# Kernel optimization log

Hardware: AMD Instinct MI355X
Metric: run time of the kernel (lower is better)

Reference implementation:

```python
import jax, jax.numpy as jnp
import numpy as np

HEADS = 16
D_MODEL = 1024
MAX_LEN = 1024
BATCH = 4
SEQ = 1024


def _skew(QEr):
    # Transformer-XL / Music-Transformer skew trick.
    # QEr: [B, H, L, L] -> pad one zero column on the left, reshape, drop first row.
    B, H, L, _ = QEr.shape
    padded = jnp.pad(QEr, ((0, 0), (0, 0), (0, 0), (1, 0)))  # [B,H,L,L+1]
    reshaped = padded.reshape(B, H, L + 1, L)
    return reshaped[:, :, 1:, :]  # [B,H,L,L]


def setup_inputs() -> dict:
    key = jax.random.key(0)
    ks = jax.random.split(key, 8)
    d = D_MODEL // HEADS
    std = 0.05  # tf.random_normal_initializer default stddev
    return {
        "query": jax.random.normal(ks[0], (BATCH, SEQ, D_MODEL), jnp.float32),
        "key": jax.random.normal(ks[1], (BATCH, SEQ, D_MODEL), jnp.float32),
        "value": jax.random.normal(ks[2], (BATCH, SEQ, D_MODEL), jnp.float32),
        "WQ": std * jax.random.normal(ks[3], (D_MODEL, D_MODEL), jnp.float32),
        "WK": std * jax.random.normal(ks[4], (D_MODEL, D_MODEL), jnp.float32),
        "WV": std * jax.random.normal(ks[5], (D_MODEL, D_MODEL), jnp.float32),
        "Er": std * jax.random.normal(ks[6], (MAX_LEN, d), jnp.float32),
        "WMerge": std * jax.random.normal(ks[7], (D_MODEL, D_MODEL), jnp.float32),
    }


def reference(query, key, value, WQ, WK, WV, Er, WMerge):
    B, L, D = query.shape
    H = HEADS
    d = D // H
    # Faithful to source: plain reshape (NOT transpose-based head split).
    q = (query @ WQ).reshape(B, H, L, d)          # [B,H,L,d]
    k_t = (key @ WK).reshape(B, H, d, L)          # [B,H,d,L]
    v = (value @ WV).reshape(B, H, L, d)          # [B,H,L,d]
    start = MAX_LEN - L
    Er_t = Er[start:, :].T                        # [d, L]
    QEr = q @ Er_t                                # [B,H,L,L]
    Srel = _skew(QEr)                             # [B,H,L,L]
    attn = (q @ k_t + Srel) / jnp.sqrt(jnp.asarray(d, q.dtype))
    attn = jax.nn.softmax(attn, axis=-1)
    out = attn @ v                                # [B,H,L,d]
    out = out.transpose(0, 2, 1, 3).reshape(B, L, D)
    return out @ WMerge
```

## Files before the change

### kernel.cpp

```cpp
#include <hip/hip_runtime.h>

#define H_  16
#define L_  1024
#define D_  1024
#define DH  64

typedef short bf16x8 __attribute__((ext_vector_type(8)));
typedef float f32x4  __attribute__((ext_vector_type(4)));

__device__ __forceinline__ ushort f2bf(float f) {
  union { float f; unsigned int u; } x; x.f = f;
  unsigned int u = x.u;
  u = (u + 0x7fffu + ((u >> 16) & 1u)) >> 16;
  return (ushort)u;
}
__device__ __forceinline__ float bf2f(ushort s) {
  union { unsigned int u; float f; } x; x.u = ((unsigned int)s) << 16;
  return x.f;
}

__device__ __forceinline__ unsigned int pkbf(float a, float b) {
  union { float f; unsigned int u; } xa, xb; xa.f = a; xb.f = b;
  unsigned int ua = xa.u + 0x8000u;
  unsigned int ub = xb.u + 0x8000u;
  return (ua >> 16) | (ub & 0xffff0000u);
}
__device__ __forceinline__ ushort lo16(unsigned int v) { return (ushort)v; }
__device__ __forceinline__ ushort hi16(unsigned int v) { return (ushort)(v >> 16); }

__device__ __forceinline__ int SZ(int F) { return F ^ (((F >> 12) & 3) << 4); }

__device__ __forceinline__ size_t afi(int m, int k) {
  return (((size_t)((m >> 7) * 32 + (k >> 5)) * 8 + ((m >> 4) & 7)) << 9)
       + ((size_t)((((k >> 3) & 3) << 4) + (m & 15)) << 3) + (k & 7);
}

__device__ __forceinline__ void gl_lds16(const ushort* g, ushort* l) {
  __builtin_amdgcn_global_load_lds(
      (const __attribute__((address_space(1))) void*)g,
      (__attribute__((address_space(3))) void*)l, 16, 0, 0);
}

__global__ __launch_bounds__(256) void prep_kernel(
    const float* __restrict__ q, const float* __restrict__ k, const float* __restrict__ v,
    ushort* __restrict__ qb, ushort* __restrict__ kb, ushort* __restrict__ vb,
    const float* __restrict__ W0, const float* __restrict__ W1,
    const float* __restrict__ W2, const float* __restrict__ W3,
    ushort* __restrict__ T0, ushort* __restrict__ T1,
    ushort* __restrict__ T2, ushort* __restrict__ T3,
    const float* __restrict__ Er, ushort* __restrict__ ErF) {
  const int bx = blockIdx.x;
  const int tid = threadIdx.x;
  if (bx < 6144) {
    const int z = bx >> 11;
    const int inner = bx & 2047;
    const float* in = (z == 0) ? q : (z == 1) ? k : v;
    ushort* out = (z == 0) ? qb : (z == 1) ? kb : vb;
    const int wv = inner * 4 + (tid >> 6);
    const int l  = tid & 63;
    const int am = wv & 7, kb2 = (wv >> 3) & 31, mb = wv >> 8;
    const int m  = mb * 128 + am * 16 + (l & 15);
    const int kk = kb2 * 32 + (l >> 4) * 8;
    float4 f0 = *(const float4*)(in + (size_t)m * 1024 + kk);
    float4 f1 = *(const float4*)(in + (size_t)m * 1024 + kk + 4);
    uint4 o;
    o.x = pkbf(f0.x, f0.y); o.y = pkbf(f0.z, f0.w);
    o.z = pkbf(f1.x, f1.y); o.w = pkbf(f1.z, f1.w);
    *(uint4*)(out + ((size_t)wv << 9) + l * 8) = o;
  } else if (bx < 7168) {
    __shared__ ushort tt[64][72];
    const int b = bx - 6144;
    const int z = b >> 8;
    const int rem = b & 255;
    const int k0 = (rem >> 4) * 64, n0 = (rem & 15) * 64;
    const float* W = (z == 0) ? W0 : (z == 1) ? W1 : (z == 2) ? W2 : W3;
    ushort*     WT = (z == 0) ? T0 : (z == 1) ? T1 : (z == 2) ? T2 : T3;
    const int t = tid;
#pragma unroll
    for (int c = 0; c < 4; ++c) {
      int kk = c * 16 + (t >> 4);
      float4 f = *(const float4*)(W + (size_t)(k0 + kk) * 1024 + n0 + (t & 15) * 4);
      unsigned int p01 = pkbf(f.x, f.y), p23 = pkbf(f.z, f.w);
      tt[(t & 15) * 4 + 0][kk] = lo16(p01);
      tt[(t & 15) * 4 + 1][kk] = hi16(p01);
      tt[(t & 15) * 4 + 2][kk] = lo16(p23);
      tt[(t & 15) * 4 + 3][kk] = hi16(p23);
    }
    __syncthreads();
#pragma unroll
    for (int p = 0; p < 2; ++p) {
      int n = p * 32 + (t >> 3);
      *(uint4*)(WT + afi(n0 + n, k0 + (t & 7) * 8)) = *(const uint4*)(&tt[n][(t & 7) * 8]);
    }
  } else {
    int t = (bx - 7168) * 256 + tid;
    int lane = t & 63, ph = (t >> 6) & 1, jg = t >> 7;
    int m = jg * 16 + (lane & 15);
    int kk = ph * 32 + (lane >> 4) * 8;
    float4 f0 = *(const float4*)(Er + m * 64 + kk);
    float4 f1 = *(const float4*)(Er + m * 64 + kk + 4);
    uint4 o;
    o.x = pkbf(f0.x, f0.y); o.y = pkbf(f0.z, f0.w);
    o.z = pkbf(f1.x, f1.y); o.w = pkbf(f1.z, f1.w);
    *(uint4*)(ErF + t * 8) = o;
  }
}

__global__ __launch_bounds__(256) void gemm_qkv_kernel(
    const ushort* __restrict__ Aq, const ushort* __restrict__ Ak, const ushort* __restrict__ Av,
    const ushort* __restrict__ BTq, const ushort* __restrict__ BTk, const ushort* __restrict__ BTv,
    ushort* __restrict__ Cq, ushort* __restrict__ Ck, ushort* __restrict__ Cv) {
  __shared__ ushort lsA[4096];
  __shared__ ushort lsB[4096];
  const int z = blockIdx.z;
  const ushort* A  = (z == 0) ? Aq  : (z == 1) ? Ak  : Av;
  const ushort* BT = (z == 0) ? BTq : (z == 1) ? BTk : BTv;
  ushort*       Cp = (z == 0) ? Cq  : (z == 1) ? Ck  : Cv;

  const int tid  = threadIdx.x;
  const int w    = tid >> 6, lane = tid & 63, qd = lane >> 4, ln = lane & 15;
  const int rw   = w >> 1, cw = w & 1;
  const int mb   = blockIdx.y, nb = blockIdx.x;
  const int m0   = mb * 128, n0 = nb * 128;

  f32x4 acc[16];
#pragma unroll
  for (int i = 0; i < 16; ++i) acc[i] = (f32x4){0.f, 0.f, 0.f, 0.f};

  for (int kb = 0; kb < 32; ++kb) {
    const ushort* Ab = A  + ((size_t)(mb * 32 + kb) << 12);
    const ushort* Bb = BT + ((size_t)(nb * 32 + kb) << 12);
    const int c0 = 2 * w;
    gl_lds16(Ab + ((size_t)c0 << 9) + lane * 8,        lsA + (c0 << 9));
    gl_lds16(Ab + ((size_t)(c0 + 1) << 9) + lane * 8,  lsA + ((c0 + 1) << 9));
    gl_lds16(Bb + ((size_t)c0 << 9) + lane * 8,        lsB + (c0 << 9));
    gl_lds16(Bb + ((size_t)(c0 + 1) << 9) + lane * 8,  lsB + ((c0 + 1) << 9));
    __syncthreads();
    bf16x8 afr[4], bfr[4];
#pragma unroll
    for (int am = 0; am < 4; ++am)
      afr[am] = *(const bf16x8*)(lsA + ((rw * 4 + am) << 9) + lane * 8);
#pragma unroll
    for (int bn = 0; bn < 4; ++bn)
      bfr[bn] = *(const bf16x8*)(lsB + ((cw * 4 + bn) << 9) + lane * 8);
#pragma unroll
    for (int am = 0; am < 4; ++am)
#pragma unroll
      for (int bn = 0; bn < 4; ++bn)
        acc[am * 4 + bn] = __builtin_amdgcn_mfma_f32_16x16x32_bf16(afr[am], bfr[bn], acc[am * 4 + bn], 0, 0, 0);
    __syncthreads();
  }
#pragma unroll
  for (int am = 0; am < 4; ++am)
#pragma unroll
    for (int bn = 0; bn < 4; ++bn) {
      const int rbase = m0 + rw * 64 + am * 16 + qd * 4;
      const int colg  = n0 + cw * 64 + bn * 16 + ln;
      const unsigned int p01 = pkbf(acc[am * 4 + bn][0], acc[am * 4 + bn][1]);
      const unsigned int p23 = pkbf(acc[am * 4 + bn][2], acc[am * 4 + bn][3]);
      if (z == 0) {
        Cp[(size_t)(rbase + 0) * 1024 + colg] = lo16(p01);
        Cp[(size_t)(rbase + 1) * 1024 + colg] = hi16(p01);
        Cp[(size_t)(rbase + 2) * 1024 + colg] = lo16(p23);
        Cp[(size_t)(rbase + 3) * 1024 + colg] = hi16(p23);
      } else if (z == 1) {
        const int bh  = rbase >> 6;
        const int ki0 = rbase & 63;
        const int jg  = colg >> 4;
        const int ph  = ki0 >> 5;
        const int lanep = ((ki0 >> 3) & 3) * 16 + (colg & 15);
        const int jj0 = ki0 & 7;
        uint2 uu; uu.x = p01; uu.y = p23;
        *(uint2*)(Cp + (size_t)bh * 65536 + (size_t)((jg * 2 + ph) * 64 + lanep) * 8 + jj0) = uu;
      } else {
        const int bh = rbase >> 6;
        const int llow = colg >> 6, dd = colg & 63;
        const int g = dd >> 4, lnf = dd & 15;
        const ushort vals[4] = {lo16(p01), hi16(p01), lo16(p23), hi16(p23)};
#pragma unroll
        for (int r = 0; r < 4; ++r) {
          int l = ((rbase + r) & 63) * 16 + llow;
          int ks = l >> 5;
          int lanep = ((l >> 3) & 3) * 16 + lnf;
          int jj = l & 7;
          Cp[(size_t)bh * 65536 + (size_t)((g * 32 + ks) * 64 + lanep) * 8 + jj] = vals[r];
        }
      }
    }
}

__global__ __launch_bounds__(256) void gemm_mg_kernel(const ushort* __restrict__ A,
                                                      const ushort* __restrict__ BT,
                                                      float* __restrict__ Cp) {
  __shared__ ushort lsA[4096];
  __shared__ ushort lsB[4096];
  const int tid  = threadIdx.x;
  const int w    = tid >> 6, lane = tid & 63, qd = lane >> 4, ln = lane & 15;
  const int rw   = w >> 1, cw = w & 1;
  const int mb   = blockIdx.y, nb = blockIdx.x, kh = blockIdx.z;
  const int m0   = mb * 128, n0 = nb * 128;

  f32x4 acc[16];
#pragma unroll
  for (int i = 0; i < 16; ++i) acc[i] = (f32x4){0.f, 0.f, 0.f, 0.f};

  for (int kb = 0; kb < 16; ++kb) {
    const int kbi = kh * 16 + kb;
    const ushort* Ab = A  + ((size_t)(mb * 32 + kbi) << 12);
    const ushort* Bb = BT + ((size_t)(nb * 32 + kbi) << 12);
    const int c0 = 2 * w;
    gl_lds16(Ab + ((size_t)c0 << 9) + lane * 8,        lsA + (c0 << 9));
    gl_lds16(Ab + ((size_t)(c0 + 1) << 9) + lane * 8,  lsA + ((c0 + 1) << 9));
    gl_lds16(Bb + ((size_t)c0 << 9) + lane * 8,        lsB + (c0 << 9));
    gl_lds16(Bb + ((size_t)(c0 + 1) << 9) + lane * 8,  lsB + ((c0 + 1) << 9));
    __syncthreads();
    bf16x8 afr[4], bfr[4];
#pragma unroll
    for (int am = 0; am < 4; ++am)
      afr[am] = *(const bf16x8*)(lsA + ((rw * 4 + am) << 9) + lane * 8);
#pragma unroll
    for (int bn = 0; bn < 4; ++bn)
      bfr[bn] = *(const bf16x8*)(lsB + ((cw * 4 + bn) << 9) + lane * 8);
#pragma unroll
    for (int am = 0; am < 4; ++am)
#pragma unroll
      for (int bn = 0; bn < 4; ++bn)
        acc[am * 4 + bn] = __builtin_amdgcn_mfma_f32_16x16x32_bf16(afr[am], bfr[bn], acc[am * 4 + bn], 0, 0, 0);
    __syncthreads();
  }

#pragma unroll
  for (int am = 0; am < 4; ++am)
#pragma unroll
    for (int bn = 0; bn < 4; ++bn) {
      const int rbase = m0 + rw * 64 + am * 16 + qd * 4;
      const int colg  = n0 + cw * 64 + bn * 16 + ln;
#pragma unroll
      for (int r = 0; r < 4; ++r)
        atomicAdd(&Cp[(size_t)(rbase + r) * 1024 + colg], acc[am * 4 + bn][r]);
    }
}

__global__ __launch_bounds__(512, 4) void attn_kernel(
    const ushort* __restrict__ QW, const ushort* __restrict__ KF,
    const ushort* __restrict__ VF, const ushort* __restrict__ ErF,
    ushort* __restrict__ Om) {
  __shared__ ushort qflat[17440];
  __shared__ float  red[4][64][4];
  __shared__ float  stats[8][16];

  const int tid  = threadIdx.x;
  const int w    = tid >> 6;
  const int lane = tid & 63;
  const int qd   = lane >> 4;
  const int ln   = lane & 15;
  const int bh   = blockIdx.y;
  const int i0   = blockIdx.x << 4;
  const ushort* q  = QW + ((size_t)bh << 16);
  const ushort* kf = KF + ((size_t)bh << 16);
  const ushort* vf = VF + ((size_t)bh << 16);

  if (tid < 17) qflat[SZ(tid * 1025 + 1024)] = 0;

  bf16x8 a00 = *(const bf16x8*)(q + (size_t)(i0 + ln) * 64 + qd * 8);
  bf16x8 a01 = *(const bf16x8*)(q + (size_t)(i0 + ln) * 64 + 32 + qd * 8);
  const int row16 = (i0 + 16 > 1023) ? 1023 : i0 + 16;
  bf16x8 a10 = *(const bf16x8*)(q + (size_t)row16 * 64 + qd * 8);
  bf16x8 a11 = *(const bf16x8*)(q + (size_t)row16 * 64 + 32 + qd * 8);

  const int jg0 = w * 8;

#pragma unroll
  for (int f = 0; f < 8; ++f) {
    const int jg = jg0 + f;
    bf16x8 b0 = *(const bf16x8*)(ErF + (size_t)((jg * 2 + 0) * 64 + lane) * 8);
    bf16x8 b1 = *(const bf16x8*)(ErF + (size_t)((jg * 2 + 1) * 64 + lane) * 8);
    f32x4 acc = {0.f, 0.f, 0.f, 0.f};
    acc = __builtin_amdgcn_mfma_f32_16x16x32_bf16(a00, b0, acc, 0, 0, 0);
    acc = __builtin_amdgcn_mfma_f32_16x16x32_bf16(a01, b1, acc, 0, 0, 0);
    const int m = jg * 16 + ln;
    const unsigned int p01 = pkbf(acc[0], acc[1]);
    const unsigned int p23 = pkbf(acc[2], acc[3]);
    qflat[SZ((qd * 4 + 0) * 1025 + m)] = lo16(p01);
    qflat[SZ((qd * 4 + 1) * 1025 + m)] = hi16(p01);
    qflat[SZ((qd * 4 + 2) * 1025 + m)] = lo16(p23);
    qflat[SZ((qd * 4 + 3) * 1025 + m)] = hi16(p23);
    if (jg * 16 <= 1006 - i0) {
      f32x4 ac2 = {0.f, 0.f, 0.f, 0.f};
      ac2 = __builtin_amdgcn_mfma_f32_16x16x32_bf16(a10, b0, ac2, 0, 0, 0);
      ac2 = __builtin_amdgcn_mfma_f32_16x16x32_bf16(a11, b1, ac2, 0, 0, 0);
      if (qd == 0) qflat[SZ(16 * 1025 + m)] = f2bf(ac2[0]);
    }
  }

  f32x4 sfr[8];
#pragma unroll
  for (int f = 0; f < 8; ++f) {
    const int jg = jg0 + f;
    bf16x8 b0 = *(const bf16x8*)(kf + (size_t)((jg * 2 + 0) * 64 + lane) * 8);
    bf16x8 b1 = *(const bf16x8*)(kf + (size_t)((jg * 2 + 1) * 64 + lane) * 8);
    f32x4 acc = {0.f, 0.f, 0.f, 0.f};
    acc = __builtin_amdgcn_mfma_f32_16x16x32_bf16(a00, b0, acc, 0, 0, 0);
    acc = __builtin_amdgcn_mfma_f32_16x16x32_bf16(a01, b1, acc, 0, 0, 0);
    sfr[f] = acc;
  }
  __syncthreads();

#pragma unroll
  for (int f = 0; f < 8; ++f) {
    const int cj = 1023 - i0 + w * 128 + f * 16 + ln;
#pragma unroll
    for (int r = 0; r < 4; ++r)
      sfr[f][r] += bf2f(qflat[SZ((qd * 4 + r) * 1024 + cj)]);
  }
  __syncthreads();

  const float cexp = 0.18033688011112042f;
  float vs[4] = {0.f, 0.f, 0.f, 0.f};
#pragma unroll
  for (int f = 0; f < 8; ++f) {
    const int j = w * 128 + f * 16 + ln;
    const float e0 = exp2f(sfr[f][0] * cexp);
    const float e1 = exp2f(sfr[f][1] * cexp);
    const float e2 = exp2f(sfr[f][2] * cexp);
    const float e3 = exp2f(sfr[f][3] * cexp);
    vs[0] += e0; vs[1] += e1; vs[2] += e2; vs[3] += e3;
    const unsigned int p01 = pkbf(e0, e1);
    const unsigned int p23 = pkbf(e2, e3);
    qflat[(qd * 4 + 0) * 1048 + j] = lo16(p01);
    qflat[(qd * 4 + 1) * 1048 + j] = hi16(p01);
    qflat[(qd * 4 + 2) * 1048 + j] = lo16(p23);
    qflat[(qd * 4 + 3) * 1048 + j] = hi16(p23);
  }
#pragma unroll
  for (int r = 0; r < 4; ++r) {
    float s = vs[r];
#pragma unroll
    for (int off = 1; off < 16; off <<= 1) s += __shfl_xor(s, off, 64);
    if (ln == 0) stats[w][qd * 4 + r] = s;
  }
  __syncthreads();
  float rrl[4];
#pragma unroll
  for (int r = 0; r < 4; ++r) {
    float s = 0.f;
#pragma unroll
    for (int ww = 0; ww < 8; ++ww) s += stats[ww][qd * 4 + r];
    rrl[r] = 1.0f / s;
  }

  const int g = w & 3, kh = w >> 2;
  f32x4 oacc0 = {0.f, 0.f, 0.f, 0.f};
  f32x4 oacc1 = {0.f, 0.f, 0.f, 0.f};
#pragma unroll
  for (int kc = 0; kc < 16; kc += 2) {
    const int ks0 = kh * 16 + kc;
    const int ks1 = ks0 + 1;
    bf16x8 ap0 = *(const bf16x8*)(qflat + ln * 1048 + ks0 * 32 + qd * 8);
    bf16x8 bv0 = *(const bf16x8*)(vf + (size_t)((g * 32 + ks0) * 64 + lane) * 8);
    oacc0 = __builtin_amdgcn_mfma_f32_16x16x32_bf16(ap0, bv0, oacc0, 0, 0, 0);
    bf16x8 ap1 = *(const bf16x8*)(qflat + ln * 1048 + ks1 * 32 + qd * 8);
    bf16x8 bv1 = *(const bf16x8*)(vf + (size_t)((g * 32 + ks1) * 64 + lane) * 8);
    oacc1 = __builtin_amdgcn_mfma_f32_16x16x32_bf16(ap1, bv1, oacc1, 0, 0, 0);
  }
  f32x4 oacc = oacc0 + oacc1;

  if (w >= 4) {
#pragma unroll
    for (int cc = 0; cc < 4; ++cc) red[w - 4][lane][cc] = oacc[cc];
  }
  __syncthreads();
  if (w < 4) {
    const int b = bh >> 4, h = bh & 15;
    const int kg = h * 64 + g * 16 + ln;
    const int mbase = b * 1024 + i0;
    ushort* ob = Om + (((size_t)((mbase >> 7) * 32 + (kg >> 5)) * 8 + ((mbase >> 4) & 7)) << 9)
               + ((((kg >> 3) & 3) * 16 + qd * 4) << 3) + (kg & 7);
    const float o0 = (oacc[0] + red[w][lane][0]) * rrl[0];
    const float o1 = (oacc[1] + red[w][lane][1]) * rrl[1];
    const float o2 = (oacc[2] + red[w][lane][2]) * rrl[2];
    const float o3 = (oacc[3] + red[w][lane][3]) * rrl[3];
    const unsigned int p01 = pkbf(o0, o1);
    const unsigned int p23 = pkbf(o2, o3);
    ob[0]  = lo16(p01);
    ob[8]  = hi16(p01);
    ob[16] = lo16(p23);
    ob[24] = hi16(p23);
  }
}

extern "C" void kernel_launch(void* const* d_in, const int* in_sizes, int n_in,
                              void* d_out, int out_size, void* d_ws, size_t ws_size,
                              hipStream_t stream) {
  const float* query = (const float*)d_in[0];
  const float* key   = (const float*)d_in[1];
  const float* value = (const float*)d_in[2];
  const float* WQ    = (const float*)d_in[3];
  const float* WK    = (const float*)d_in[4];
  const float* WV    = (const float*)d_in[5];
  const float* Er    = (const float*)d_in[6];
  const float* WM    = (const float*)d_in[7];
  float* out = (float*)d_out;

  ushort* QW  = (ushort*)d_ws;
  ushort* KF  = QW  + (size_t)4096 * 1024;
  ushort* VF  = KF  + (size_t)4096 * 1024;
  ushort* O   = VF  + (size_t)4096 * 1024;
  ushort* ErF = O   + (size_t)4096 * 1024;
  ushort* WTQ = ErF + (size_t)65536;
  ushort* WTK = WTQ + (size_t)1024 * 1024;
  ushort* WTV = WTK + (size_t)1024 * 1024;
  ushort* WTM = WTV + (size_t)1024 * 1024;
  ushort* KB  = WTM + (size_t)1024 * 1024;
  ushort* VB  = KB  + (size_t)4096 * 1024;
  ushort* QB  = O;

  hipMemsetAsync(out, 0, (size_t)4096 * 1024 * sizeof(float), stream);

  prep_kernel<<<7200, 256, 0, stream>>>(query, key, value, QB, KB, VB,
                                        WQ, WK, WV, WM, WTQ, WTK, WTV, WTM,
                                        Er, ErF);

  gemm_qkv_kernel<<<dim3(8, 32, 3), 256, 0, stream>>>(QB, KB, VB,
                                                      WTQ, WTK, WTV,
                                                      QW, KF, VF);

  attn_kernel<<<dim3(64, 64), 512, 0, stream>>>(QW, KF, VF, ErF, O);

  gemm_mg_kernel<<<dim3(8, 32, 2), 256, 0, stream>>>(O, WTM, out);
}
```

Before: 276.4 us.

## Replace split-K atomics in merge GEMM with 64-row tiles and direct stores

The output-projection GEMM no longer splits K across two blocks that combine results with float atomicAdd. Each block now covers 64 rows by 128 columns over the full K range, which keeps the block count the same, and writes results with plain stores. Because no block accumulates into the output anymore, the memset that zeroed it is removed. This avoids atomic traffic and one memset launch, at the cost of a longer K loop per block and uneven global-to-LDS load work across waves.

```diff
diff --git a/kernel.cpp b/kernel.cpp
--- a/kernel.cpp
+++ b/kernel.cpp
@@ -192,37 +192,49 @@
 __global__ __launch_bounds__(256) void gemm_mg_kernel(const ushort* __restrict__ A,
                                                       const ushort* __restrict__ BT,
                                                       float* __restrict__ Cp) {
-  __shared__ ushort lsA[4096];
+  __shared__ ushort lsA[2048];
   __shared__ ushort lsB[4096];
   const int tid  = threadIdx.x;
   const int w    = tid >> 6, lane = tid & 63, qd = lane >> 4, ln = lane & 15;
   const int rw   = w >> 1, cw = w & 1;
-  const int mb   = blockIdx.y, nb = blockIdx.x, kh = blockIdx.z;
-  const int m0   = mb * 128, n0 = nb * 128;
-
-  f32x4 acc[16];
-#pragma unroll
-  for (int i = 0; i < 16; ++i) acc[i] = (f32x4){0.f, 0.f, 0.f, 0.f};
-
-  for (int kb = 0; kb < 16; ++kb) {
-    const int kbi = kh * 16 + kb;
-    const ushort* Ab = A  + ((size_t)(mb * 32 + kbi) << 12);
-    const ushort* Bb = BT + ((size_t)(nb * 32 + kbi) << 12);
-    const int c0 = 2 * w;
-    gl_lds16(Ab + ((size_t)c0 << 9) + lane * 8,        lsA + (c0 << 9));
-    gl_lds16(Ab + ((size_t)(c0 + 1) << 9) + lane * 8,  lsA + ((c0 + 1) << 9));
-    gl_lds16(Bb + ((size_t)c0 << 9) + lane * 8,        lsB + (c0 << 9));
-    gl_lds16(Bb + ((size_t)(c0 + 1) << 9) + lane * 8,  lsB + ((c0 + 1) << 9));
+  const int mb   = blockIdx.y, nb = blockIdx.x;
+  const int m0   = mb * 64, n0 = nb * 128;
+  const int amo  = (mb & 1) * 4;
+
+  f32x4 acc[8];
+#pragma unroll
+  for (int i = 0; i < 8; ++i) acc[i] = (f32x4){0.f, 0.f, 0.f, 0.f};
+
+  for (int kb = 0; kb < 32; ++kb) {
+    const ushort* Ab = A  + ((size_t)((mb >> 1) * 32 + kb) << 12);
+    const ushort* Bb = BT + ((size_t)(nb * 32 + kb) << 12);
+    if (w == 0) {
+      gl_lds16(Ab + ((size_t)(amo + 0) << 9) + lane * 8, lsA + (0 << 9));
+      gl_lds16(Ab + ((size_t)(amo + 1) << 9) + lane * 8, lsA + (1 << 9));
+      gl_lds16(Ab + ((size_t)(amo + 2) << 9) + lane * 8, lsA + (2 << 9));
+    } else if (w == 1) {
+      gl_lds16(Ab + ((size_t)(amo + 3) << 9) + lane * 8, lsA + (3 << 9));
+      gl_lds16(Bb + ((size_t)0 << 9) + lane * 8,         lsB + (0 << 9));
+      gl_lds16(Bb + ((size_t)1 << 9) + lane * 8,         lsB + (1 << 9));
+    } else if (w == 2) {
+      gl_lds16(Bb + ((size_t)2 << 9) + lane * 8,         lsB + (2 << 9));
+      gl_lds16(Bb + ((size_t)3 << 9) + lane * 8,         lsB + (3 << 9));
+      gl_lds16(Bb + ((size_t)4 << 9) + lane * 8,         lsB + (4 << 9));
+    } else {
+      gl_lds16(Bb + ((size_t)5 << 9) + lane * 8,         lsB + (5 << 9));
+      gl_lds16(Bb + ((size_t)6 << 9) + lane * 8,         lsB + (6 << 9));
+      gl_lds16(Bb + ((size_t)7 << 9) + lane * 8,         lsB + (7 << 9));
+    }
     __syncthreads();
-    bf16x8 afr[4], bfr[4];
-#pragma unroll
-    for (int am = 0; am < 4; ++am)
-      afr[am] = *(const bf16x8*)(lsA + ((rw * 4 + am) << 9) + lane * 8);
+    bf16x8 afr[2], bfr[4];
+#pragma unroll
+    for (int am = 0; am < 2; ++am)
+      afr[am] = *(const bf16x8*)(lsA + ((rw * 2 + am) << 9) + lane * 8);
 #pragma unroll
     for (int bn = 0; bn < 4; ++bn)
       bfr[bn] = *(const bf16x8*)(lsB + ((cw * 4 + bn) << 9) + lane * 8);
 #pragma unroll
-    for (int am = 0; am < 4; ++am)
+    for (int am = 0; am < 2; ++am)
 #pragma unroll
       for (int bn = 0; bn < 4; ++bn)
         acc[am * 4 + bn] = __builtin_amdgcn_mfma_f32_16x16x32_bf16(afr[am], bfr[bn], acc[am * 4 + bn], 0, 0, 0);
@@ -230,14 +242,14 @@
   }
 
 #pragma unroll
-  for (int am = 0; am < 4; ++am)
+  for (int am = 0; am < 2; ++am)
 #pragma unroll
     for (int bn = 0; bn < 4; ++bn) {
-      const int rbase = m0 + rw * 64 + am * 16 + qd * 4;
+      const int rbase = m0 + rw * 32 + am * 16 + qd * 4;
       const int colg  = n0 + cw * 64 + bn * 16 + ln;
 #pragma unroll
       for (int r = 0; r < 4; ++r)
-        atomicAdd(&Cp[(size_t)(rbase + r) * 1024 + colg], acc[am * 4 + bn][r]);
+        Cp[(size_t)(rbase + r) * 1024 + colg] = acc[am * 4 + bn][r];
     }
 }
 
@@ -415,8 +427,6 @@
   ushort* VB  = KB  + (size_t)4096 * 1024;
   ushort* QB  = O;
 
-  hipMemsetAsync(out, 0, (size_t)4096 * 1024 * sizeof(float), stream);
-
   prep_kernel<<<7200, 256, 0, stream>>>(query, key, value, QB, KB, VB,
                                         WQ, WK, WV, WM, WTQ, WTK, WTV, WTM,
                                         Er, ErF);
@@ -427,5 +437,5 @@
 
   attn_kernel<<<dim3(64, 64), 512, 0, stream>>>(QW, KF, VF, ErF, O);
 
-  gemm_mg_kernel<<<dim3(8, 32, 2), 256, 0, stream>>>(O, WTM, out);
-}
+  gemm_mg_kernel<<<dim3(8, 64), 256, 0, stream>>>(O, WTM, out);
+}
```

New measurement: 257.9 us. 1.07x faster.
